# Optimization experiments

Measured on AMD Instinct MI355X. Metric: run time of the kernel, lower is better.

The kernel has to match this reference:

```python
import jax, jax.numpy as jnp
import numpy as np

DECAY = 0.99
EPS = 1e-5
COMMIT = 0.25

def setup_inputs() -> dict:
    key = jax.random.key(0)
    k1, k2 = jax.random.split(key)
    inputs = jax.random.normal(k1, (2, 64, 48, 48, 48), dtype=jnp.float32)
    emb_weight = jax.random.normal(k2, (256, 64), dtype=jnp.float32)
    return {
        "inputs": inputs,
        "emb_weight": emb_weight,
        "ema_cluster_size": jnp.zeros((256,), jnp.float32),
        "ema_w": emb_weight.copy(),  # registered buffer initialized as clone of embedding
    }

def reference(inputs, emb_weight, ema_cluster_size, ema_w):
    B, C, D, H, W = inputs.shape
    K = emb_weight.shape[0]
    # quantize: channel-last flatten [B*D*H*W, C]
    flat_input = jnp.transpose(inputs, (0, 2, 3, 4, 1)).reshape(-1, C)
    # pairwise squared distances via norms + matmul
    distances = ((flat_input ** 2).sum(axis=1, keepdims=True)
                 + (emb_weight ** 2).sum(axis=1)[None, :]
                 - 2.0 * flat_input @ emb_weight.T)  # [N, K]
    encoding_indices = jnp.argmin(distances, axis=1)  # [N]
    # embed: gather codebook rows, reshape to channel-first [B, C, D, H, W]
    quantized = jnp.transpose(emb_weight[encoding_indices].reshape(B, D, H, W, C), (0, 4, 1, 2, 3))
    # EMA codebook update (training branch; one-hot sums expressed as segment reductions)
    encodings_sum = jax.ops.segment_sum(jnp.ones(flat_input.shape[0], jnp.float32), encoding_indices, num_segments=K)
    dw = jax.ops.segment_sum(flat_input, encoding_indices, num_segments=K)  # [K, C]
    new_cluster_size = DECAY * ema_cluster_size + (1.0 - DECAY) * encodings_sum
    n = new_cluster_size.sum()
    weights = (new_cluster_size + EPS) / (n + K * EPS) * n
    new_ema_w = DECAY * ema_w + (1.0 - DECAY) * dw
    new_emb_weight = new_ema_w / weights[:, None]
    # commitment loss (quantized detached) scaled by 10, straight-through estimator
    loss = COMMIT * jnp.mean((jax.lax.stop_gradient(quantized) - inputs) ** 2) * 10.0
    quantized_out = inputs + jax.lax.stop_gradient(quantized - inputs)
    enc_idx = encoding_indices.reshape(B, D, H, W)
    return (quantized_out, loss, enc_idx, encodings_sum, new_emb_weight)
```

## Files before the change

### kernel.cpp

```cpp
#include <hip/hip_runtime.h>
#include <hip/hip_bf16.h>

#define SPA 110592
#define NPOS 221184
#define NELEM 14155776
#define KCODES 256
#define CCH 64
#define PBLK 512
#define PPOS 432
#define DWBLK 432
#define DWTHR 512
#define EPS_TIE 0.0625f

typedef __attribute__((ext_vector_type(8))) short bf16x8;
typedef __attribute__((ext_vector_type(16))) float f32x16;

__device__ __forceinline__ void bf16split(float v, short& h, short& l) {
    unsigned bits = __builtin_bit_cast(unsigned, v);
    h = (short)(bits >> 16);
    float hf = __builtin_bit_cast(float, bits & 0xFFFF0000u);
    float res = v - hf;
    l = (short)(__builtin_bit_cast(unsigned, res) >> 16);
}

__device__ __forceinline__ float bf16join(short h, short l) {
    float hf = __builtin_bit_cast(float, ((unsigned)(unsigned short)h) << 16);
    float lf = __builtin_bit_cast(float, ((unsigned)(unsigned short)l) << 16);
    return hf + lf;
}

__device__ __forceinline__ float dpack(float d, int k) {
    unsigned bits = (__builtin_bit_cast(unsigned, d) & 0xFFFFFF00u) | (unsigned)k;
    return __builtin_bit_cast(float, bits);
}
__device__ __forceinline__ int dkey(float d) {
    return (int)(__builtin_bit_cast(unsigned, d) & 0xFFu);
}

__device__ __forceinline__ void top2merge(float& m1, float& m2, float o1, float o2) {
    float a = fminf(m1, o1);
    float b = fmaxf(m1, o1);
    m2 = fminf(b, fminf(m2, o2));
    m1 = a;
}

__global__ __launch_bounds__(256) void vq_init(
    const float* __restrict__ emb, float* __restrict__ en2,
    float* __restrict__ dw, float* __restrict__ hist, float* __restrict__ loss)
{
    int t = blockIdx.x * 256 + threadIdx.x;
    if (t < CCH * KCODES) dw[t] = 0.f;
    if (t < KCODES) {
        const float* e = emb + (t << 6);
        float s = 0.f;
#pragma unroll
        for (int c = 0; c < CCH; ++c) s = fmaf(e[c], e[c], s);
        en2[t] = s;
        hist[t] = 0.f;
    }
    if (t == 0) loss[0] = 0.f;
}

__global__ __launch_bounds__(256, 4) void vq_argmin_mfma(
    const float* __restrict__ in, const float* __restrict__ emb,
    const float* __restrict__ en2, float* __restrict__ qout,
    float* __restrict__ encout, float* __restrict__ hist,
    float* __restrict__ loss)
{
    __shared__ __align__(16) short xh[8][128][8];
    __shared__ __align__(16) short xl[8][128][8];
    __shared__ float e2s[KCODES];
    __shared__ float pm1[4][128], pm2[4][128];
    __shared__ int   bestkS[128];
    __shared__ float lhist[KCODES];
    __shared__ float lred[4];

    int tid  = threadIdx.x;
    int w    = tid >> 6, lane = tid & 63;
    int hi   = lane >> 5, col = lane & 31;
    int wbase = w * 64;

    int blk = blockIdx.x;
    int b   = (blk >= 864) ? 1 : 0;
    int s0  = (blk - b * 864) * 128;
    const float* xbase = in + b * (CCH * SPA) + s0;

    if (tid < KCODES) { e2s[tid] = en2[tid]; lhist[tid] = 0.f; }

    bf16x8 Ah[2][4], Al[2][4];
#pragma unroll
    for (int ct = 0; ct < 2; ++ct) {
        int code = wbase + ct * 32 + col;
        const float* er = emb + (code << 6) + hi * 8;
#pragma unroll
        for (int j = 0; j < 4; ++j) {
            bf16x8 hfr, lfr;
#pragma unroll
            for (int jj = 0; jj < 8; ++jj) {
                short hs, ls; bf16split(er[j * 16 + jj], hs, ls);
                hfr[jj] = hs; lfr[jj] = ls;
            }
            Ah[ct][j] = hfr; Al[ct][j] = lfr;
        }
    }

    {
        int tg = tid >> 7, p = tid & 127;
        const float* xb = xbase + p;
#pragma unroll
        for (int cb = 0; cb < 4; ++cb) {
            int c0 = tg * 32 + cb * 8;
            bf16x8 hfr, lfr;
#pragma unroll
            for (int jj = 0; jj < 8; ++jj) {
                short hs, ls; bf16split(xb[(c0 + jj) * SPA], hs, ls);
                hfr[jj] = hs; lfr[jj] = ls;
            }
            *(bf16x8*)&xh[c0 >> 3][p][0] = hfr;
            *(bf16x8*)&xl[c0 >> 3][p][0] = lfr;
        }
    }
    __syncthreads();

#pragma unroll 1
    for (int pt = 0; pt < 4; ++pt) {
        int pos = pt * 32 + col;
        f32x16 c0, c1;
#pragma unroll
        for (int i = 0; i < 16; ++i) { c0[i] = 0.f; c1[i] = 0.f; }

#pragma unroll
        for (int j = 0; j < 4; ++j) {
            bf16x8 bh = *(const bf16x8*)&xh[j * 2 + hi][pos][0];
            bf16x8 bl = *(const bf16x8*)&xl[j * 2 + hi][pos][0];
            c0 = __builtin_amdgcn_mfma_f32_32x32x16_bf16(Ah[0][j], bh, c0, 0, 0, 0);
            c1 = __builtin_amdgcn_mfma_f32_32x32x16_bf16(Ah[1][j], bh, c1, 0, 0, 0);
            c0 = __builtin_amdgcn_mfma_f32_32x32x16_bf16(Ah[0][j], bl, c0, 0, 0, 0);
            c1 = __builtin_amdgcn_mfma_f32_32x32x16_bf16(Ah[1][j], bl, c1, 0, 0, 0);
            c0 = __builtin_amdgcn_mfma_f32_32x32x16_bf16(Al[0][j], bh, c0, 0, 0, 0);
            c1 = __builtin_amdgcn_mfma_f32_32x32x16_bf16(Al[1][j], bh, c1, 0, 0, 0);
        }

        float m1 = 1e30f, m2 = 1e30f;
#pragma unroll
        for (int ct = 0; ct < 2; ++ct) {
#pragma unroll
            for (int r = 0; r < 16; ++r) {
                int kc  = wbase + ct * 32 + (r & 3) + 8 * (r >> 2) + 4 * hi;
                float d = dpack(fmaf(-2.f, (ct ? c1[r] : c0[r]), e2s[kc]), kc);
                float lo  = fminf(d, m1);
                float hi2 = fmaxf(d, m1);
                m2 = fminf(hi2, m2);
                m1 = lo;
            }
        }
        top2merge(m1, m2, __shfl_xor(m1, 32, 64), __shfl_xor(m2, 32, 64));
        if (hi == 0) { pm1[w][pos] = m1; pm2[w][pos] = m2; }
    }
    __syncthreads();

    if (tid < 128) {
        int p = tid;
        float M1 = pm1[0][p], M2 = pm2[0][p];
#pragma unroll
        for (int ww = 1; ww < 4; ++ww)
            top2merge(M1, M2, pm1[ww][p], pm2[ww][p]);
        int K1 = dkey(M1), K2 = dkey(M2);
        int bk = K1;
        if (M2 <= M1 + EPS_TIE) {
            int ka = min(K1, K2), kb = max(K1, K2);
            const float* xb2 = xbase + p;
            const float* ea  = emb + (ka << 6);
            const float* eb2 = emb + (kb << 6);
            float da = 0.f, db = 0.f;
#pragma unroll 4
            for (int c = 0; c < CCH; ++c) {
                float xv = xb2[c * SPA];
                da = fmaf(xv, ea[c], da);
                db = fmaf(xv, eb2[c], db);
            }
            float Da = e2s[ka] - 2.f * da;
            float Db = e2s[kb] - 2.f * db;
            bk = (Db < Da) ? kb : ka;
        }
        bestkS[p] = bk;
        encout[b * SPA + s0 + p] = (float)bk;
        atomicAdd(&lhist[bk], 1.0f);
    }
    __syncthreads();

    {
        int tg = tid >> 7, p = tid & 127;
        int k = bestkS[p];
        const float* ee = emb + (k << 6) + tg * 32;
        float* qp = qout + b * (CCH * SPA) + s0 + p;
        float lsum = 0.f;
#pragma unroll
        for (int cb = 0; cb < 4; ++cb) {
            int oct = tg * 4 + cb;
            bf16x8 hfr = *(const bf16x8*)&xh[oct][p][0];
            bf16x8 lfr = *(const bf16x8*)&xl[oct][p][0];
#pragma unroll
            for (int jj = 0; jj < 8; ++jj) {
                float xv = bf16join(hfr[jj], lfr[jj]);
                float q  = ee[cb * 8 + jj];
                float d  = q - xv;
                lsum = fmaf(d, d, lsum);
                qp[(tg * 32 + cb * 8 + jj) * SPA] = q;
            }
        }
        for (int off = 32; off > 0; off >>= 1) lsum += __shfl_down(lsum, off, 64);
        if (lane == 0) lred[w] = lsum;
    }
    __syncthreads();
    if (tid == 0)
        unsafeAtomicAdd(loss, (lred[0] + lred[1] + lred[2] + lred[3]) * (2.5f / 14155776.f));
    if (tid < KCODES && lhist[tid] != 0.f)
        unsafeAtomicAdd(&hist[tid], lhist[tid]);
}

__global__ __launch_bounds__(512) void vq_dw_part(
    const float* __restrict__ in, const float* __restrict__ encout,
    float* __restrict__ partial)
{
    __shared__ float l[CCH * KCODES];
    int tid = threadIdx.x;
#pragma unroll
    for (int i = tid; i < CCH * KCODES; i += 512) l[i] = 0.f;
    __syncthreads();

    if (tid < PPOS) {
        int n = blockIdx.x * PPOS + tid;
        int b = (n >= SPA) ? 1 : 0;
        int s = n - b * SPA;
        int k = (int)encout[n];
        const float* xp = in + b * (CCH * SPA) + s;
#pragma unroll
        for (int c = 0; c < CCH; ++c)
            atomicAdd(&l[(c << 8) + (k ^ (c & 31))], xp[c * SPA]);
    }
    __syncthreads();

    float* pp = partial + (size_t)blockIdx.x * (CCH * KCODES);
#pragma unroll
    for (int i = tid; i < CCH * KCODES; i += 512) {
        int k2 = i >> 6, c = i & 63;
        pp[i] = l[(c << 8) + (k2 ^ (c & 31))];
    }
}

__global__ __launch_bounds__(256) void vq_dw_reduce(
    const float* __restrict__ partial, float* __restrict__ dw)
{
    __shared__ float acc[4][64];
    int t = threadIdx.x, lane6 = t & 63, tsub = t >> 6;
    int i = blockIdx.x * 64 + lane6;
    float s = 0.f;
    for (int p = tsub * 128; p < tsub * 128 + 128; ++p)
        s += partial[(size_t)p * (CCH * KCODES) + i];
    acc[tsub][lane6] = s;
    __syncthreads();
    if (tsub == 0)
        dw[i] = (acc[0][lane6] + acc[1][lane6]) + (acc[2][lane6] + acc[3][lane6]);
}

__global__ __launch_bounds__(DWTHR) void vq_dw_atomic(
    const float* __restrict__ in, const float* __restrict__ encout,
    float* __restrict__ dw)
{
    __shared__ float l[CCH * KCODES];
    int tid = threadIdx.x;
    for (int i = tid; i < CCH * KCODES; i += DWTHR) l[i] = 0.f;
    __syncthreads();
    int n = blockIdx.x * DWTHR + tid;
    int b = (n >= SPA) ? 1 : 0;
    int s = n - b * SPA;
    int k = (int)encout[n];
    const float* xp = in + b * (CCH * SPA) + s;
#pragma unroll
    for (int c = 0; c < CCH; ++c)
        atomicAdd(&l[(c << 8) + (k ^ (c & 31))], xp[c * SPA]);
    __syncthreads();
    for (int i = tid; i < CCH * KCODES; i += DWTHR) {
        int k2 = i >> 6, c = i & 63;
        unsafeAtomicAdd(&dw[i], l[(c << 8) + (k2 ^ (c & 31))]);
    }
}

__global__ __launch_bounds__(256) void vq_ema_w(
    const float* __restrict__ csize, const float* __restrict__ hist,
    float* __restrict__ wbuf)
{
    __shared__ float red[KCODES];
    int t = threadIdx.x;
    float ncs = 0.99f * csize[t] + 0.01f * hist[t];
    red[t] = ncs;
    __syncthreads();
    for (int off = 128; off > 0; off >>= 1) {
        if (t < off) red[t] += red[t + off];
        __syncthreads();
    }
    float nsum = red[0];
    wbuf[t] = (ncs + 1e-5f) / (nsum + 256.f * 1e-5f) * nsum;
}

__global__ __launch_bounds__(256) void vq_emb(
    const float* __restrict__ emaw, const float* __restrict__ dw,
    const float* __restrict__ wbuf, float* __restrict__ embo)
{
    int i = blockIdx.x * 256 + threadIdx.x;
    float nw = fmaf(0.01f, dw[i], 0.99f * emaw[i]);
    embo[i] = nw / wbuf[i >> 6];
}

extern "C" void kernel_launch(void* const* d_in, const int* in_sizes, int n_in,
                              void* d_out, int out_size, void* d_ws, size_t ws_size,
                              hipStream_t stream)
{
    const float* in   = (const float*)d_in[0];
    const float* emb  = (const float*)d_in[1];
    const float* cs   = (const float*)d_in[2];
    const float* emaw = (const float*)d_in[3];

    float* out  = (float*)d_out;
    float* qout = out;
    float* loss = out + NELEM;
    float* enc  = loss + 1;
    float* hist = enc + NPOS;
    float* embo = hist + KCODES;

    float* en2     = (float*)d_ws;
    float* wbuf    = en2 + KCODES;
    float* dw      = wbuf + KCODES;
    float* partial = dw + CCH * KCODES;

    size_t need = (size_t)(2 * KCODES + CCH * KCODES) * 4
                + (size_t)PBLK * CCH * KCODES * 4;
    bool use_part = (ws_size >= need);

    vq_init<<<dim3(64), dim3(256), 0, stream>>>(emb, en2, dw, hist, loss);
    vq_argmin_mfma<<<dim3(1728), dim3(256), 0, stream>>>(in, emb, en2, qout, enc, hist, loss);
    if (use_part) {
        vq_dw_part<<<dim3(PBLK), dim3(512), 0, stream>>>(in, enc, partial);
        vq_dw_reduce<<<dim3(256), dim3(256), 0, stream>>>(partial, dw);
    } else {
        vq_dw_atomic<<<dim3(DWBLK), dim3(DWTHR), 0, stream>>>(in, enc, dw);
    }
    vq_ema_w<<<dim3(1), dim3(256), 0, stream>>>(cs, hist, wbuf);
    vq_emb<<<dim3(64), dim3(256), 0, stream>>>(emaw, dw, wbuf, embo);
}
```

Baseline: 275.8 us.

## Precompute codebook bf16 fragments once, halve dW partials, fuse EMA kernels

The bf16 hi/lo split of the codebook moves out of every argmin block into vq_init, which writes fragment arrays that each block loads directly, and the codebook-norm computation is parallelised with shuffles. The dW partial pass now uses 256 blocks of 864 positions, which halves the partial buffer and the reduce traffic. The two tail EMA kernels are merged into one 1024-thread launch. The argmin launch bound drops to 3 waves per SIMD, which changes register allocation and may lower occupancy.

```diff
diff --git a/kernel.cpp b/kernel.cpp
--- a/kernel.cpp
+++ b/kernel.cpp
@@ -6,8 +6,8 @@
 #define NELEM 14155776
 #define KCODES 256
 #define CCH 64
-#define PBLK 512
-#define PPOS 432
+#define NPART 256
+#define PPB 864
 #define DWBLK 432
 #define DWTHR 512
 #define EPS_TIE 0.0625f
@@ -46,24 +46,46 @@
 
 __global__ __launch_bounds__(256) void vq_init(
     const float* __restrict__ emb, float* __restrict__ en2,
-    float* __restrict__ dw, float* __restrict__ hist, float* __restrict__ loss)
+    float* __restrict__ dw, float* __restrict__ hist, float* __restrict__ loss,
+    float* __restrict__ fragH, float* __restrict__ fragL)
 {
     int t = blockIdx.x * 256 + threadIdx.x;
     if (t < CCH * KCODES) dw[t] = 0.f;
-    if (t < KCODES) {
-        const float* e = emb + (t << 6);
+    if (t < 2048) {
+        int g = t >> 6, lane = t & 63;
+        int w = g >> 3, ct = (g >> 2) & 1, j = g & 3;
+        int code = w * 64 + ct * 32 + (lane & 31);
+        int ch0 = (lane >> 5) * 8 + j * 16;
+        const float* er = emb + (code << 6) + ch0;
+        bf16x8 hfr, lfr;
+#pragma unroll
+        for (int jj = 0; jj < 8; ++jj) {
+            short hs, ls; bf16split(er[jj], hs, ls);
+            hfr[jj] = hs; lfr[jj] = ls;
+        }
+        ((bf16x8*)fragH)[t] = hfr;
+        ((bf16x8*)fragL)[t] = lfr;
+    }
+    if (t >= 2048 && t < 4096) {
+        int t2 = t - 2048;
+        int code = t2 >> 3, seg = t2 & 7;
+        const float* e = emb + (code << 6) + seg * 8;
         float s = 0.f;
 #pragma unroll
-        for (int c = 0; c < CCH; ++c) s = fmaf(e[c], e[c], s);
-        en2[t] = s;
-        hist[t] = 0.f;
-    }
+        for (int jj = 0; jj < 8; ++jj) s = fmaf(e[jj], e[jj], s);
+        s += __shfl_down(s, 4, 64);
+        s += __shfl_down(s, 2, 64);
+        s += __shfl_down(s, 1, 64);
+        if (seg == 0) en2[code] = s;
+    }
+    if (t < KCODES) hist[t] = 0.f;
     if (t == 0) loss[0] = 0.f;
 }
 
-__global__ __launch_bounds__(256, 4) void vq_argmin_mfma(
+__global__ __launch_bounds__(256, 3) void vq_argmin_mfma(
     const float* __restrict__ in, const float* __restrict__ emb,
-    const float* __restrict__ en2, float* __restrict__ qout,
+    const float* __restrict__ en2, const float* __restrict__ fragH,
+    const float* __restrict__ fragL, float* __restrict__ qout,
     float* __restrict__ encout, float* __restrict__ hist,
     float* __restrict__ loss)
 {
@@ -87,22 +109,17 @@
 
     if (tid < KCODES) { e2s[tid] = en2[tid]; lhist[tid] = 0.f; }
 
+    const bf16x8* fH = (const bf16x8*)fragH;
+    const bf16x8* fL = (const bf16x8*)fragL;
     bf16x8 Ah[2][4], Al[2][4];
 #pragma unroll
-    for (int ct = 0; ct < 2; ++ct) {
-        int code = wbase + ct * 32 + col;
-        const float* er = emb + (code << 6) + hi * 8;
+    for (int ct = 0; ct < 2; ++ct)
 #pragma unroll
         for (int j = 0; j < 4; ++j) {
-            bf16x8 hfr, lfr;
-#pragma unroll
-            for (int jj = 0; jj < 8; ++jj) {
-                short hs, ls; bf16split(er[j * 16 + jj], hs, ls);
-                hfr[jj] = hs; lfr[jj] = ls;
-            }
-            Ah[ct][j] = hfr; Al[ct][j] = lfr;
-        }
-    }
+            int g = (w * 8 + ct * 4 + j) * 64 + lane;
+            Ah[ct][j] = fH[g];
+            Al[ct][j] = fL[g];
+        }
 
     {
         int tg = tid >> 7, p = tid & 127;
@@ -229,9 +246,19 @@
     for (int i = tid; i < CCH * KCODES; i += 512) l[i] = 0.f;
     __syncthreads();
 
-    if (tid < PPOS) {
-        int n = blockIdx.x * PPOS + tid;
-        int b = (n >= SPA) ? 1 : 0;
+    int base = blockIdx.x * PPB;
+    int b    = (blockIdx.x >= 128) ? 1 : 0;
+    {
+        int n = base + tid;
+        int s = n - b * SPA;
+        int k = (int)encout[n];
+        const float* xp = in + b * (CCH * SPA) + s;
+#pragma unroll
+        for (int c = 0; c < CCH; ++c)
+            atomicAdd(&l[(c << 8) + (k ^ (c & 31))], xp[c * SPA]);
+    }
+    if (tid < PPB - 512) {
+        int n = base + 512 + tid;
         int s = n - b * SPA;
         int k = (int)encout[n];
         const float* xp = in + b * (CCH * SPA) + s;
@@ -256,7 +283,7 @@
     int t = threadIdx.x, lane6 = t & 63, tsub = t >> 6;
     int i = blockIdx.x * 64 + lane6;
     float s = 0.f;
-    for (int p = tsub * 128; p < tsub * 128 + 128; ++p)
+    for (int p = tsub * 64; p < tsub * 64 + 64; ++p)
         s += partial[(size_t)p * (CCH * KCODES) + i];
     acc[tsub][lane6] = s;
     __syncthreads();
@@ -287,30 +314,28 @@
     }
 }
 
-__global__ __launch_bounds__(256) void vq_ema_w(
-    const float* __restrict__ csize, const float* __restrict__ hist,
-    float* __restrict__ wbuf)
+__global__ __launch_bounds__(1024) void vq_ema(
+    const float* __restrict__ csize, const float* __restrict__ emaw,
+    const float* __restrict__ hist, const float* __restrict__ dw,
+    float* __restrict__ embo)
 {
     __shared__ float red[KCODES];
+    __shared__ float wsm[KCODES];
     int t = threadIdx.x;
-    float ncs = 0.99f * csize[t] + 0.01f * hist[t];
-    red[t] = ncs;
+    float ncs = 0.f;
+    if (t < KCODES) { ncs = 0.99f * csize[t] + 0.01f * hist[t]; red[t] = ncs; }
     __syncthreads();
     for (int off = 128; off > 0; off >>= 1) {
         if (t < off) red[t] += red[t + off];
         __syncthreads();
     }
     float nsum = red[0];
-    wbuf[t] = (ncs + 1e-5f) / (nsum + 256.f * 1e-5f) * nsum;
-}
-
-__global__ __launch_bounds__(256) void vq_emb(
-    const float* __restrict__ emaw, const float* __restrict__ dw,
-    const float* __restrict__ wbuf, float* __restrict__ embo)
-{
-    int i = blockIdx.x * 256 + threadIdx.x;
-    float nw = fmaf(0.01f, dw[i], 0.99f * emaw[i]);
-    embo[i] = nw / wbuf[i >> 6];
+    if (t < KCODES) wsm[t] = (ncs + 1e-5f) / (nsum + 256.f * 1e-5f) * nsum;
+    __syncthreads();
+    for (int i = t; i < CCH * KCODES; i += 1024) {
+        float nw = fmaf(0.01f, dw[i], 0.99f * emaw[i]);
+        embo[i] = nw / wsm[i >> 6];
+    }
 }
 
 extern "C" void kernel_launch(void* const* d_in, const int* in_sizes, int n_in,
@@ -330,22 +355,23 @@
     float* embo = hist + KCODES;
 
     float* en2     = (float*)d_ws;
-    float* wbuf    = en2 + KCODES;
-    float* dw      = wbuf + KCODES;
-    float* partial = dw + CCH * KCODES;
-
-    size_t need = (size_t)(2 * KCODES + CCH * KCODES) * 4
-                + (size_t)PBLK * CCH * KCODES * 4;
+    float* dw      = en2 + KCODES;
+    float* fragH   = dw + CCH * KCODES;
+    float* fragL   = fragH + 8192;
+    float* partial = fragL + 8192;
+
+    size_t need = (size_t)(KCODES + CCH * KCODES + 16384) * 4
+                + (size_t)NPART * CCH * KCODES * 4;
     bool use_part = (ws_size >= need);
 
-    vq_init<<<dim3(64), dim3(256), 0, stream>>>(emb, en2, dw, hist, loss);
-    vq_argmin_mfma<<<dim3(1728), dim3(256), 0, stream>>>(in, emb, en2, qout, enc, hist, loss);
+    vq_init<<<dim3(64), dim3(256), 0, stream>>>(emb, en2, dw, hist, loss, fragH, fragL);
+    vq_argmin_mfma<<<dim3(1728), dim3(256), 0, stream>>>(in, emb, en2, fragH, fragL,
+                                                         qout, enc, hist, loss);
     if (use_part) {
-        vq_dw_part<<<dim3(PBLK), dim3(512), 0, stream>>>(in, enc, partial);
+        vq_dw_part<<<dim3(NPART), dim3(512), 0, stream>>>(in, enc, partial);
         vq_dw_reduce<<<dim3(256), dim3(256), 0, stream>>>(partial, dw);
     } else {
         vq_dw_atomic<<<dim3(DWBLK), dim3(DWTHR), 0, stream>>>(in, enc, dw);
     }
-    vq_ema_w<<<dim3(1), dim3(256), 0, stream>>>(cs, hist, wbuf);
-    vq_emb<<<dim3(64), dim3(256), 0, stream>>>(emaw, dw, wbuf, embo);
-}
+    vq_ema<<<dim3(1), dim3(1024), 0, stream>>>(cs, emaw, hist, dw, embo);
+}
```

After: 274.5 us. About the same (-0.5%).
